# Performance work log

Measured on AMD Instinct MI355X. Metric: run time of the kernel, lower is better.

The kernel has to match this reference:

```python
import jax, jax.numpy as jnp
import numpy as np
from jax import lax

DIM, HF, WF = 768, 14, 8   # h = H, w = W//2 + 1
B, H, W = 128, 14, 14
EPS = 1e-5


def setup_inputs() -> dict:
    key = jax.random.key(0)
    k = jax.random.split(key, 5)
    half = DIM // 2
    return {
        "x": jax.random.normal(k[0], (B, DIM, H, W), dtype=jnp.float32),
        "dw_weight": jax.random.normal(k[1], (half, 1, 3, 3), dtype=jnp.float32) * 0.1,
        "complex_weight": jax.random.normal(k[2], (half, HF, WF, 2), dtype=jnp.float32) * 0.02,
        "proj_weight": jax.random.normal(k[3], (DIM, DIM, 1, 1), dtype=jnp.float32) * 0.02,
        "proj_bias": jnp.zeros((DIM,), dtype=jnp.float32),
        "bn_gamma": jnp.ones((DIM,), dtype=jnp.float32),
        "bn_beta": jnp.zeros((DIM,), dtype=jnp.float32),
    }


def reference(x, dw_weight, complex_weight, proj_weight, proj_bias, bn_gamma, bn_beta):
    half = x.shape[1] // 2
    x1, x2 = x[:, :half], x[:, half:]

    # depthwise 3x3 conv, padding=1, no bias
    x1 = lax.conv_general_dilated(
        x1, dw_weight, window_strides=(1, 1), padding="SAME",
        dimension_numbers=("NCHW", "OIHW", "NCHW"), feature_group_count=half)

    # spectral filter: rfft2 -> complex elementwise multiply -> irfft2 (ortho norm)
    x2_fft = jnp.fft.rfft2(x2, norm="ortho")               # [B, half, H, W//2+1]
    w_fft = complex_weight[..., 0] + 1j * complex_weight[..., 1]  # [half, h, w]
    x2_filt = jnp.fft.irfft2(x2_fft * w_fft, s=(x2.shape[-2], x2.shape[-1]), norm="ortho")

    out = jnp.concatenate((x1, x2_filt), axis=1)           # [B, DIM, H, W]

    # 1x1 projection conv with bias (a GEMM over channels)
    w = proj_weight[:, :, 0, 0]                            # [DIM, DIM]
    out = jnp.einsum("bchw,oc->bohw", out, w) + proj_bias[None, :, None, None]

    # BatchNorm2d, training mode (batch statistics over N,H,W)
    mean = jnp.mean(out, axis=(0, 2, 3), keepdims=True)
    var = jnp.var(out, axis=(0, 2, 3), keepdims=True)
    out = (out - mean) * lax.rsqrt(var + EPS)
    out = out * bn_gamma[None, :, None, None] + bn_beta[None, :, None, None]
    return out
```

## Files before the change

### kernel.cpp

```cpp
#include <hip/hip_runtime.h>

typedef __attribute__((ext_vector_type(8))) __bf16 bf16x8;
typedef __attribute__((ext_vector_type(4))) float f32x4;

#define B_    128
#define DIM_  768
#define HALF_ 384
#define HW_   196
#define NPOS_ (B_*HW_)
#define IMG_  (DIM_*HW_)

typedef const __attribute__((address_space(1))) void* gas_t;
typedef __attribute__((address_space(3))) void* las_t;

__device__ __forceinline__ unsigned short f2bf(float f) {
  unsigned int u = __builtin_bit_cast(unsigned int, f);
  u = (u + 0x7FFFu + ((u >> 16) & 1u)) >> 16;
  return (unsigned short)u;
}

__global__ void k_zero(float* __restrict__ stats) {
  int i = blockIdx.x * 256 + threadIdx.x;
  if (i < 2 * DIM_) stats[i] = 0.f;
}

__global__ void k_wspatial(const float* __restrict__ cw, float* __restrict__ wsp) {
  __shared__ float ct[14], st[14];
  const int c = blockIdx.x;
  const int tid = threadIdx.x;
  if (tid < 14) {
    float s, co;
    sincosf(0.44879895051282760549f * (float)tid, &s, &co);
    ct[tid] = co; st[tid] = s;
  }
  __syncthreads();
  const int y = tid / 14, xx = tid % 14;
  float acc = 0.f;
  for (int u = 0; u < 14; ++u) {
    #pragma unroll
    for (int v = 0; v < 8; ++v) {
      int idx = (u * y + v * xx) % 14;
      float wr = cw[(((size_t)c * 14 + u) * 8 + v) * 2 + 0];
      float wi = cw[(((size_t)c * 14 + u) * 8 + v) * 2 + 1];
      float fac = (v == 0 || v == 7) ? 1.f : 2.f;
      acc += fac * (wr * ct[idx] - wi * st[idx]);
    }
  }
  wsp[(size_t)c * 196 + tid] = acc * (1.f / 196.f);
}

__global__ void k_cvtW(const float* __restrict__ pw, unsigned short* __restrict__ Wb) {
  int i = blockIdx.x * 256 + threadIdx.x;
  float4 v = reinterpret_cast<const float4*>(pw)[i];
  unsigned int lo = (unsigned int)f2bf(v.x) | ((unsigned int)f2bf(v.y) << 16);
  unsigned int hi = (unsigned int)f2bf(v.z) | ((unsigned int)f2bf(v.w) << 16);
  reinterpret_cast<uint2*>(Wb)[i] = make_uint2(lo, hi);
}

__global__ __launch_bounds__(256) void k_dwconv(
    const float* __restrict__ x, const float* __restrict__ dww,
    unsigned short* __restrict__ featT) {
  __shared__ __align__(16) float xin[16][196];
  __shared__ float wgt[16][9];
  __shared__ __align__(16) unsigned short outT[196][16];
  const int cgrp = blockIdx.x;
  const int b = blockIdx.y;
  const int c0 = cgrp * 16;
  const int tid = threadIdx.x;

  for (int i = tid; i < 16 * 196; i += 256)
    xin[i / 196][i % 196] = x[(size_t)b * IMG_ + (size_t)(c0 + i / 196) * 196 + (i % 196)];
  if (tid < 144) wgt[tid / 9][tid % 9] = dww[(size_t)c0 * 9 + tid];
  __syncthreads();

  if (tid < 224) {
    const int cc = tid / 14;
    const int y0 = tid % 14;
    float w00 = wgt[cc][0], w01 = wgt[cc][1], w02 = wgt[cc][2];
    float w10 = wgt[cc][3], w11 = wgt[cc][4], w12 = wgt[cc][5];
    float w20 = wgt[cc][6], w21 = wgt[cc][7], w22 = wgt[cc][8];
    #pragma unroll
    for (int xx = 0; xx < 14; ++xx) {
      float acc = 0.f;
      #pragma unroll
      for (int ky = 0; ky < 3; ++ky) {
        int yy = y0 + ky - 1;
        bool yok = (yy >= 0) && (yy <= 13);
        #pragma unroll
        for (int kx = 0; kx < 3; ++kx) {
          int xs = xx + kx - 1;
          if (xs < 0 || xs > 13) continue;
          float wv = (ky == 0) ? (kx == 0 ? w00 : kx == 1 ? w01 : w02)
                   : (ky == 1) ? (kx == 0 ? w10 : kx == 1 ? w11 : w12)
                               : (kx == 0 ? w20 : kx == 1 ? w21 : w22);
          if (yok) acc += xin[cc][yy * 14 + xs] * wv;
        }
      }
      outT[y0 * 14 + xx][cc] = f2bf(acc);
    }
  }
  __syncthreads();
  for (int i = tid; i < 196 * 16; i += 256) {
    int pix = i >> 4, cc = i & 15;
    featT[(size_t)(b * 196 + pix) * DIM_ + (c0 + cc)] = outT[pix][cc];
  }
}

__global__ __launch_bounds__(256) void k_circmm(
    const float* __restrict__ x, const float* __restrict__ wsp,
    unsigned short* __restrict__ feat2) {
  __shared__ __align__(16) unsigned short As[128 * 72];
  __shared__ __align__(16) unsigned short Bs[208 * 72];
  const int c = blockIdx.x;
  const int tid = threadIdx.x;
  const int lane = tid & 63;
  const int wv = tid >> 6;
  const int fr = lane & 15, fg = lane >> 4;
  const float* xc = x + (size_t)(HALF_ + c) * 196;
  const float* wspc = wsp + (size_t)c * 196;

  f32x4 acc[2][13];
  #pragma unroll
  for (int mi = 0; mi < 2; ++mi)
    #pragma unroll
    for (int ni = 0; ni < 13; ++ni) acc[mi][ni] = (f32x4)0.0f;

  for (int kt = 0; kt < 4; ++kt) {
    for (int i = tid; i < 2048; i += 256) {
      int b = i >> 4, jj = i & 15;
      int k = kt * 64 + jj * 4;
      ushort4 st = {0, 0, 0, 0};
      if (k < 196) {
        float4 v = *reinterpret_cast<const float4*>(xc + (size_t)b * IMG_ + k);
        st.x = f2bf(v.x); st.y = f2bf(v.y); st.z = f2bf(v.z); st.w = f2bf(v.w);
      }
      *reinterpret_cast<ushort4*>(&As[b * 72 + jj * 4]) = st;
    }
    for (int i = tid; i < 12544; i += 256) {
      int po = i >> 6, kl = i & 63;
      int pi = kt * 64 + kl;
      unsigned short w = 0;
      if (pi < 196) {
        int yo = po / 14, xo = po - yo * 14;
        int yi = pi / 14, xi = pi - yi * 14;
        int dy = yo - yi; dy += (dy >> 31) & 14;
        int dx = xo - xi; dx += (dx >> 31) & 14;
        w = f2bf(wspc[dy * 14 + dx]);
      }
      Bs[po * 72 + kl] = w;
    }
    __syncthreads();
    #pragma unroll
    for (int ks = 0; ks < 64; ks += 32) {
      bf16x8 a0 = *reinterpret_cast<const bf16x8*>(&As[(wv * 32 + fr) * 72 + ks + fg * 8]);
      bf16x8 a1 = *reinterpret_cast<const bf16x8*>(&As[(wv * 32 + 16 + fr) * 72 + ks + fg * 8]);
      #pragma unroll
      for (int ni = 0; ni < 13; ++ni) {
        bf16x8 bv = *reinterpret_cast<const bf16x8*>(&Bs[(ni * 16 + fr) * 72 + ks + fg * 8]);
        acc[0][ni] = __builtin_amdgcn_mfma_f32_16x16x32_bf16(a0, bv, acc[0][ni], 0, 0, 0);
        acc[1][ni] = __builtin_amdgcn_mfma_f32_16x16x32_bf16(a1, bv, acc[1][ni], 0, 0, 0);
      }
    }
    __syncthreads();
  }

  unsigned short* f2c = feat2 + (size_t)c * NPOS_;
  #pragma unroll
  for (int mi = 0; mi < 2; ++mi) {
    int b0 = wv * 32 + mi * 16 + fg * 4;
    #pragma unroll
    for (int ni = 0; ni < 13; ++ni) {
      int p = ni * 16 + fr;
      if (p < 196) {
        #pragma unroll
        for (int j = 0; j < 4; ++j)
          f2c[(size_t)(b0 + j) * 196 + p] = f2bf(acc[mi][ni][j]);
      }
    }
  }
}

__global__ __launch_bounds__(256) void k_tr(
    const unsigned short* __restrict__ feat2, unsigned short* __restrict__ featT) {
  __shared__ __align__(16) unsigned short T2[64 * 264];
  const int n0 = blockIdx.x * 256;
  const int c0 = blockIdx.y * 64;
  const int tid = threadIdx.x;

  #pragma unroll
  for (int p = 0; p < 8; ++p) {
    int i = tid + p * 256;
    int c_l = i >> 5, nj = i & 31;
    uint4 v = *reinterpret_cast<const uint4*>(feat2 + (size_t)(c0 + c_l) * NPOS_ + n0 + nj * 8);
    *reinterpret_cast<uint4*>(&T2[c_l * 264 + nj * 8]) = v;
  }
  __syncthreads();
  #pragma unroll
  for (int p = 0; p < 8; ++p) {
    int i = tid + p * 256;
    int n_l = i >> 3, cj = i & 7;
    unsigned short vs[8];
    #pragma unroll
    for (int k = 0; k < 8; ++k) vs[k] = T2[(cj * 8 + k) * 264 + n_l];
    uint4 o;
    o.x = (unsigned int)vs[0] | ((unsigned int)vs[1] << 16);
    o.y = (unsigned int)vs[2] | ((unsigned int)vs[3] << 16);
    o.z = (unsigned int)vs[4] | ((unsigned int)vs[5] << 16);
    o.w = (unsigned int)vs[6] | ((unsigned int)vs[7] << 16);
    *reinterpret_cast<uint4*>(featT + (size_t)(n0 + n_l) * DIM_ + HALF_ + c0 + cj * 8) = o;
  }
}

__global__ __launch_bounds__(256) void k_gemm(
    const unsigned short* __restrict__ Wb, const unsigned short* __restrict__ featT,
    const float* __restrict__ bias, float* __restrict__ y, float* __restrict__ stats) {
  __shared__ __align__(16) unsigned short As[128 * 64];
  __shared__ __align__(16) unsigned short Bs[128 * 64];

  const int bx = blockIdx.x;
  const int by = blockIdx.y;
  const int tid = threadIdx.x;
  const int lane = tid & 63;
  const int wave = tid >> 6;
  const int wm = wave >> 1;
  const int wn = wave & 1;
  const int o_blk = by * 128;
  const int n_blk = bx * 128;
  const int fr = lane & 15, fg = lane >> 4;

  const unsigned short* sA[4];
  const unsigned short* sB[4];
  int ldsOff[4];
  #pragma unroll
  for (int i = 0; i < 4; ++i) {
    int chunk = i * 256 + tid;
    int r = chunk >> 3;
    int j = chunk & 7;
    int srcCol = (j ^ (r & 7)) << 3;
    sA[i] = Wb    + (size_t)(o_blk + r) * 768 + srcCol;
    sB[i] = featT + (size_t)(n_blk + r) * 768 + srcCol;
    ldsOff[i] = chunk << 3;
  }

  int offA[2][4], offB[2][4];
  #pragma unroll
  for (int mi = 0; mi < 4; ++mi) {
    int row = wm * 64 + mi * 16 + fr;
    offA[0][mi] = (row << 6) + (((fg)     ^ (row & 7)) << 3);
    offA[1][mi] = (row << 6) + (((fg + 4) ^ (row & 7)) << 3);
  }
  #pragma unroll
  for (int ni = 0; ni < 4; ++ni) {
    int row = wn * 64 + ni * 16 + fr;
    offB[0][ni] = (row << 6) + (((fg)     ^ (row & 7)) << 3);
    offB[1][ni] = (row << 6) + (((fg + 4) ^ (row & 7)) << 3);
  }

  f32x4 acc[4][4];
  #pragma unroll
  for (int i = 0; i < 4; ++i)
    #pragma unroll
    for (int j = 0; j < 4; ++j) acc[i][j] = (f32x4)0.0f;

  for (int kt = 0; kt < 768; kt += 64) {
    #pragma unroll
    for (int i = 0; i < 4; ++i) {
      __builtin_amdgcn_global_load_lds((gas_t)(sA[i] + kt), (las_t)(&As[ldsOff[i]]), 16, 0, 0);
      __builtin_amdgcn_global_load_lds((gas_t)(sB[i] + kt), (las_t)(&Bs[ldsOff[i]]), 16, 0, 0);
    }
    asm volatile("s_waitcnt vmcnt(0)" ::: "memory");
    __syncthreads();
    #pragma unroll
    for (int half = 0; half < 2; ++half) {
      bf16x8 af[4], bfv[4];
      #pragma unroll
      for (int mi = 0; mi < 4; ++mi)
        af[mi] = *reinterpret_cast<const bf16x8*>(&As[offA[half][mi]]);
      #pragma unroll
      for (int ni = 0; ni < 4; ++ni)
        bfv[ni] = *reinterpret_cast<const bf16x8*>(&Bs[offB[half][ni]]);
      #pragma unroll
      for (int mi = 0; mi < 4; ++mi)
        #pragma unroll
        for (int ni = 0; ni < 4; ++ni)
          acc[mi][ni] = __builtin_amdgcn_mfma_f32_16x16x32_bf16(af[mi], bfv[ni], acc[mi][ni], 0, 0, 0);
    }
    __syncthreads();
  }

  const int col_l = lane & 15;
  #pragma unroll
  for (int mi = 0; mi < 4; ++mi) {
    const int o0 = o_blk + wm * 64 + mi * 16 + (lane >> 4) * 4;
    float bs[4], sv[4], s2v[4];
    #pragma unroll
    for (int j = 0; j < 4; ++j) { bs[j] = bias[o0 + j]; sv[j] = 0.f; s2v[j] = 0.f; }
    #pragma unroll
    for (int ni = 0; ni < 4; ++ni) {
      int n = n_blk + wn * 64 + ni * 16 + col_l;
      int b = n / 196;
      int hw = n % 196;
      size_t base = (size_t)b * IMG_ + (size_t)o0 * 196 + hw;
      #pragma unroll
      for (int j = 0; j < 4; ++j) {
        float v = acc[mi][ni][j] + bs[j];
        y[base + j * 196] = v;
        sv[j] += v; s2v[j] += v * v;
      }
    }
    #pragma unroll
    for (int j = 0; j < 4; ++j) {
      float a = sv[j], q = s2v[j];
      #pragma unroll
      for (int m = 1; m < 16; m <<= 1) { a += __shfl_xor(a, m); q += __shfl_xor(q, m); }
      if (col_l == 0) {
        atomicAdd(&stats[o0 + j], a);
        atomicAdd(&stats[DIM_ + o0 + j], q);
      }
    }
  }
}

__global__ __launch_bounds__(256) void k_bnapply(
    float* __restrict__ y, const float* __restrict__ stats,
    const float* __restrict__ gamma, const float* __restrict__ beta) {
  const int o = blockIdx.x;
  const int q = blockIdx.y;
  const float mean = stats[o] * (1.f / (float)NPOS_);
  const float var  = stats[DIM_ + o] * (1.f / (float)NPOS_) - mean * mean;
  const float g  = gamma[o] * rsqrtf(var + 1e-5f);
  const float be = beta[o] - mean * g;

  for (int i = threadIdx.x; i < 1568; i += 256) {
    int bl = i / 49;
    int h4 = i - bl * 49;
    float4* p = reinterpret_cast<float4*>(
        y + (size_t)(q * 32 + bl) * IMG_ + (size_t)o * 196) + h4;
    float4 v = *p;
    v.x = v.x * g + be; v.y = v.y * g + be; v.z = v.z * g + be; v.w = v.w * g + be;
    *p = v;
  }
}

extern "C" void kernel_launch(void* const* d_in, const int* in_sizes, int n_in,
                              void* d_out, int out_size, void* d_ws, size_t ws_size,
                              hipStream_t stream) {
  const float* x     = (const float*)d_in[0];
  const float* dww   = (const float*)d_in[1];
  const float* cw    = (const float*)d_in[2];
  const float* pw    = (const float*)d_in[3];
  const float* pb    = (const float*)d_in[4];
  const float* gamma = (const float*)d_in[5];
  const float* beta  = (const float*)d_in[6];
  float* out = (float*)d_out;

  char* wsb = (char*)d_ws;
  unsigned short* featT = (unsigned short*)wsb;
  unsigned short* Wb    = (unsigned short*)(wsb + 38535168);
  float* wsp            = (float*)(wsb + 39714816);
  unsigned short* feat2 = (unsigned short*)(wsb + 40015872);
  float* stats          = (float*)(wsb + 59283456);

  k_zero<<<dim3(6), dim3(256), 0, stream>>>(stats);
  k_wspatial<<<dim3(HALF_), dim3(HW_), 0, stream>>>(cw, wsp);
  k_cvtW<<<dim3(576), dim3(256), 0, stream>>>(pw, Wb);
  k_dwconv<<<dim3(24, B_), dim3(256), 0, stream>>>(x, dww, featT);
  k_circmm<<<dim3(HALF_), dim3(256), 0, stream>>>(x, wsp, feat2);
  k_tr<<<dim3(98, 6), dim3(256), 0, stream>>>(feat2, featT);
  k_gemm<<<dim3(196, 6), dim3(256), 0, stream>>>(Wb, featT, pb, out, stats);
  k_bnapply<<<dim3(DIM_, 4), dim3(256), 0, stream>>>(out, stats, gamma, beta);
}
```

Before: 394.0 us.

## Register-prefetch next GEMM tile and remap blocks across XCDs

The GEMM drops direct global-to-LDS loads in favour of loading the next K tile into registers, issued right after the barrier so the loads overlap the MFMA work on the current tile, then writing them to swizzled LDS. It also turns the 2D grid into a 1D grid and remaps block IDs so that consecutive blocks sharing B tiles land on the same XCD (pid&7 grouping), aiming for better L2 reuse. The cost is extra VGPRs for the staging registers and an additional LDS write pass.

```diff
diff --git a/kernel.cpp b/kernel.cpp
--- a/kernel.cpp
+++ b/kernel.cpp
@@ -9,9 +9,6 @@
 #define HW_   196
 #define NPOS_ (B_*HW_)
 #define IMG_  (DIM_*HW_)
-
-typedef const __attribute__((address_space(1))) void* gas_t;
-typedef __attribute__((address_space(3))) void* las_t;
 
 __device__ __forceinline__ unsigned short f2bf(float f) {
   unsigned int u = __builtin_bit_cast(unsigned int, f);
@@ -217,8 +214,11 @@
   __shared__ __align__(16) unsigned short As[128 * 64];
   __shared__ __align__(16) unsigned short Bs[128 * 64];
 
-  const int bx = blockIdx.x;
-  const int by = blockIdx.y;
+  const int pid = blockIdx.x;
+  const int logical = (pid & 7) * 147 + (pid >> 3);
+  const int bx = logical / 6;
+  const int by = logical - 6 * bx;
+
   const int tid = threadIdx.x;
   const int lane = tid & 63;
   const int wave = tid >> 6;
@@ -230,16 +230,15 @@
 
   const unsigned short* sA[4];
   const unsigned short* sB[4];
-  int ldsOff[4];
+  int dstOff[4];
   #pragma unroll
   for (int i = 0; i < 4; ++i) {
     int chunk = i * 256 + tid;
     int r = chunk >> 3;
     int j = chunk & 7;
-    int srcCol = (j ^ (r & 7)) << 3;
-    sA[i] = Wb    + (size_t)(o_blk + r) * 768 + srcCol;
-    sB[i] = featT + (size_t)(n_blk + r) * 768 + srcCol;
-    ldsOff[i] = chunk << 3;
+    sA[i] = Wb    + (size_t)(o_blk + r) * 768 + (j << 3);
+    sB[i] = featT + (size_t)(n_blk + r) * 768 + (j << 3);
+    dstOff[i] = (r << 6) + ((j ^ (r & 7)) << 3);
   }
 
   int offA[2][4], offB[2][4];
@@ -262,14 +261,27 @@
     #pragma unroll
     for (int j = 0; j < 4; ++j) acc[i][j] = (f32x4)0.0f;
 
-  for (int kt = 0; kt < 768; kt += 64) {
+  uint4 rA[4], rB[4];
+  #pragma unroll
+  for (int i = 0; i < 4; ++i) {
+    rA[i] = *reinterpret_cast<const uint4*>(sA[i]);
+    rB[i] = *reinterpret_cast<const uint4*>(sB[i]);
+  }
+
+  for (int t = 0; t < 12; ++t) {
     #pragma unroll
     for (int i = 0; i < 4; ++i) {
-      __builtin_amdgcn_global_load_lds((gas_t)(sA[i] + kt), (las_t)(&As[ldsOff[i]]), 16, 0, 0);
-      __builtin_amdgcn_global_load_lds((gas_t)(sB[i] + kt), (las_t)(&Bs[ldsOff[i]]), 16, 0, 0);
-    }
-    asm volatile("s_waitcnt vmcnt(0)" ::: "memory");
+      *reinterpret_cast<uint4*>(&As[dstOff[i]]) = rA[i];
+      *reinterpret_cast<uint4*>(&Bs[dstOff[i]]) = rB[i];
+    }
     __syncthreads();
+    if (t < 11) {
+      #pragma unroll
+      for (int i = 0; i < 4; ++i) {
+        rA[i] = *reinterpret_cast<const uint4*>(sA[i] + (t + 1) * 64);
+        rB[i] = *reinterpret_cast<const uint4*>(sB[i] + (t + 1) * 64);
+      }
+    }
     #pragma unroll
     for (int half = 0; half < 2; ++half) {
       bf16x8 af[4], bfv[4];
@@ -367,6 +379,6 @@
   k_dwconv<<<dim3(24, B_), dim3(256), 0, stream>>>(x, dww, featT);
   k_circmm<<<dim3(HALF_), dim3(256), 0, stream>>>(x, wsp, feat2);
   k_tr<<<dim3(98, 6), dim3(256), 0, stream>>>(feat2, featT);
-  k_gemm<<<dim3(196, 6), dim3(256), 0, stream>>>(Wb, featT, pb, out, stats);
+  k_gemm<<<dim3(1176), dim3(256), 0, stream>>>(Wb, featT, pb, out, stats);
   k_bnapply<<<dim3(DIM_, 4), dim3(256), 0, stream>>>(out, stats, gamma, beta);
 }
```

New measurement: 416.6 us. 5.7% more time.
